# Performance work log

Hardware: AMD Instinct MI355X
Metric: run time of the kernel (lower is better)

## Reference

```python
import jax, jax.numpy as jnp
import numpy as np
from functools import partial

B, T, D = 4, 1024, 1024
NH = 16            # n_branches
DH = D // NH       # d_branch = 64
SOMA_H = int(D * 3.0)
EPS = 1e-5

def _gelu(x):
    return jax.nn.gelu(x, approximate=False)  # torch default GELU is exact erf

def _gconv(x_cf, w, b, pad_left, groups):
    # x_cf: [B, C_in, T], w: [C_out, C_in//groups, K] (torch OIW layout)
    y = jax.lax.conv_general_dilated(
        x_cf, w, window_strides=(1,), padding=[(pad_left, 0)],
        feature_group_count=groups, dimension_numbers=('NCH', 'OIH', 'NCH'))
    return y + b[None, :, None]

def setup_inputs() -> dict:
    key = jax.random.key(0)
    ks = jax.random.split(key, 16)
    s = 0.02
    return {
        'x': jax.random.normal(ks[0], (B, T, D), jnp.float32),
        'nmda': jax.random.normal(ks[1], (B, NH, DH), jnp.float32),
        'qkv_w': jax.random.normal(ks[2], (D, 3 * D), jnp.float32) * s,
        'nmda_decay': jax.random.normal(ks[3], (1, NH, 1, DH), jnp.float32) * 0.1 + 0.9,
        'tconv_w': jax.random.normal(ks[4], (D, DH, 5), jnp.float32) * s,
        'tconv_b': jnp.zeros((D,), jnp.float32),
        'ffu_w': jax.random.normal(ks[5], (2 * D, DH, 1), jnp.float32) * s,
        'ffu_b': jnp.zeros((2 * D,), jnp.float32),
        'ffd_w': jax.random.normal(ks[6], (D, 2 * DH, 1), jnp.float32) * s,
        'ffd_b': jnp.zeros((D,), jnp.float32),
        'gn_w': jnp.ones((D,), jnp.float32),
        'gn_b': jnp.zeros((D,), jnp.float32),
        'soma_w': jax.random.normal(ks[7], (D, D), jnp.float32) * s,
        'ln_w': jnp.ones((D,), jnp.float32),
        'ln_b': jnp.zeros((D,), jnp.float32),
        'w1': jax.random.normal(ks[8], (D, SOMA_H), jnp.float32) * s,
        'b1': jnp.zeros((SOMA_H,), jnp.float32),
        'w2': jax.random.normal(ks[9], (SOMA_H, D), jnp.float32) * s,
        'b2': jnp.zeros((D,), jnp.float32),
    }

def reference(x, nmda, qkv_w, nmda_decay, tconv_w, tconv_b, ffu_w, ffu_b,
              ffd_w, ffd_b, gn_w, gn_b, soma_w, ln_w, ln_b, w1, b1, w2, b2):
    # QKV projection -> [B, T, 3, NH, DH] -> Q,K,V [B, NH, T, DH]
    qkv = (x @ qkv_w).reshape(B, T, 3, NH, DH).transpose(2, 0, 3, 1, 4)
    Q, K, V = qkv[0], qkv[1], qkv[2]
    # NMDA trace injection into V, gated by sigmoid(decay)
    tau = jax.nn.sigmoid(nmda_decay)                    # [1, NH, 1, DH]
    V = V + nmda[:, :, None, :] * tau
    # causal SDPA
    scale = 1.0 / jnp.sqrt(jnp.asarray(DH, x.dtype))
    scores = jnp.einsum('bhqd,bhkd->bhqk', Q, K) * scale
    causal = jnp.tril(jnp.ones((T, T), bool))
    scores = jnp.where(causal[None, None], scores, jnp.finfo(x.dtype).min)
    attn = jnp.einsum('bhqk,bhkd->bhqd', jax.nn.softmax(scores, axis=-1), V)
    branch_flat = attn.transpose(0, 2, 1, 3).reshape(B, T, D)   # [B,T,D]
    # causal temporal grouped conv (pad=4, k=5, truncated to T => left-pad 4)
    x_cf = branch_flat.transpose(0, 2, 1)                       # [B,D,T]
    x_cf = x_cf + _gconv(x_cf, tconv_w, tconv_b, 4, NH)
    # grouped 1x1 FFN
    ff_hidden = _gelu(_gconv(x_cf, ffu_w, ffu_b, 0, NH))        # [B,2D,T]
    ff_out = _gconv(ff_hidden, ffd_w, ffd_b, 0, NH).transpose(0, 2, 1)
    residual = branch_flat + ff_out
    # GroupNorm over each branch's DH channels (per token)
    r = residual.reshape(B, T, NH, DH)
    mu = r.mean(-1, keepdims=True)
    var = ((r - mu) ** 2).mean(-1, keepdims=True)
    normed_heads = (r - mu) / jnp.sqrt(var + EPS)
    normed_heads = normed_heads * gn_w.reshape(NH, DH) + gn_b.reshape(NH, DH)
    normed = normed_heads.reshape(B, T, D)
    # NMDA state update from last token
    branch_last = normed_heads[:, -1]                           # [B,NH,DH]
    tau2 = jax.nn.sigmoid(nmda_decay[:, :, 0, :])               # [1,NH,DH]
    new_nmda = tau2 * nmda + (1.0 - tau2) * branch_last
    # soma projection + LN + FFN (exact GELU)
    soma = normed @ soma_w
    mu2 = soma.mean(-1, keepdims=True)
    var2 = ((soma - mu2) ** 2).mean(-1, keepdims=True)
    lns = (soma - mu2) / jnp.sqrt(var2 + EPS) * ln_w + ln_b
    soma = soma + (_gelu(lns @ w1 + b1) @ w2 + b2)
    return soma, new_nmda
```

## Files before the change

### kernel.cpp

```cpp
#include <hip/hip_runtime.h>
#include <math.h>

#define B_  4
#define T_  1024
#define D_  1024
#define NH_ 16
#define DH_ 64
#define SH_ 3072

typedef unsigned short u16;
typedef __attribute__((ext_vector_type(8))) short bf16x8;
typedef __attribute__((ext_vector_type(4))) float f32x4;
typedef __attribute__((ext_vector_type(4))) unsigned short u16x4;
typedef __attribute__((ext_vector_type(8))) unsigned short u16x8;

__device__ __forceinline__ float gelu_f(float x) {
    return 0.5f * x * (1.0f + erff(x * 0.70710678118654752440f));
}
__device__ __forceinline__ float sigm_f(float x) {
    return 1.0f / (1.0f + __expf(-x));
}
__device__ __forceinline__ u16 f2bf(float f) {
    unsigned u = __builtin_bit_cast(unsigned, f);
    return (u16)((u + 0x7FFFu + ((u >> 16) & 1u)) >> 16);
}

#define GLD16(gsrc, ldst) __builtin_amdgcn_global_load_lds( \
    (__attribute__((address_space(1))) void*)(gsrc),        \
    (__attribute__((address_space(3))) void*)(ldst), 16, 0, 0)

__global__ __launch_bounds__(256) void cast_bf16_k(
    const float* __restrict__ in, u16* __restrict__ out, int n8)
{
    int i = blockIdx.x * 256 + threadIdx.x;
    if (i >= n8) return;
    const float4* p = (const float4*)(in + (size_t)i * 8);
    float4 a = p[0], b = p[1];
    u16x8 o;
    o[0] = f2bf(a.x); o[1] = f2bf(a.y); o[2] = f2bf(a.z); o[3] = f2bf(a.w);
    o[4] = f2bf(b.x); o[5] = f2bf(b.y); o[6] = f2bf(b.z); o[7] = f2bf(b.w);
    *(u16x8*)(out + (size_t)i * 8) = o;
}

__global__ __launch_bounds__(256) void transpose_cast_k(
    const float* __restrict__ W, u16* __restrict__ Wt, int K, int N)
{
    __shared__ float t[32][33];
    const int n0 = blockIdx.x * 32, k0 = blockIdx.y * 32;
    const int tid = threadIdx.x;
    {
        int kr = tid >> 3, nc = (tid & 7) * 4;
        float4 v = *(const float4*)(W + (size_t)(k0 + kr) * N + n0 + nc);
        t[kr][nc] = v.x; t[kr][nc + 1] = v.y; t[kr][nc + 2] = v.z; t[kr][nc + 3] = v.w;
    }
    __syncthreads();
    {
        int nr = tid >> 3, kc = (tid & 7) * 4;
        u16x4 o = { f2bf(t[kc][nr]), f2bf(t[kc + 1][nr]),
                    f2bf(t[kc + 2][nr]), f2bf(t[kc + 3][nr]) };
        *(u16x4*)(Wt + (size_t)(n0 + nr) * K + k0 + kc) = o;
    }
}

template<bool BIAS, bool GELU, bool ACCUM, bool BF16OUT>
__global__ __launch_bounds__(256) void gemm_mfma(
    const u16* __restrict__ A, const u16* __restrict__ Bt,
    const float* __restrict__ bias, void* __restrict__ Cv,
    int M, int N, int K)
{
    __shared__ u16 As[4096];
    __shared__ u16 Bs[4096];
    const int tid = threadIdx.x;
    const int m0 = blockIdx.y * 128, n0 = blockIdx.x * 128;
    const int w = tid >> 6, l = tid & 63;
    const int mw = (w >> 1) * 64, nw = (w & 1) * 64;
    const int lr = l & 15, kg = l >> 4;
    const int swz = kg ^ ((lr >> 1) & 3);

    f32x4 acc[4][4];
#pragma unroll
    for (int i = 0; i < 4; ++i)
#pragma unroll
        for (int j = 0; j < 4; ++j) acc[i][j] = (f32x4){0.f, 0.f, 0.f, 0.f};

    const int mA0 = tid >> 2;
    const int kg0 = (tid & 3) ^ ((mA0 >> 1) & 3);
    const int mA1 = (256 + tid) >> 2;
    const int kg1 = ((256 + tid) & 3) ^ ((mA1 >> 1) & 3);
    const u16* a0 = A + (size_t)(m0 + mA0) * K + kg0 * 8;
    const u16* a1 = A + (size_t)(m0 + mA1) * K + kg1 * 8;
    const u16* b0 = Bt + (size_t)(n0 + mA0) * K + kg0 * 8;
    const u16* b1 = Bt + (size_t)(n0 + mA1) * K + kg1 * 8;
    u16* lA0 = As + tid * 8;  u16* lA1 = As + (256 + tid) * 8;
    u16* lB0 = Bs + tid * 8;  u16* lB1 = Bs + (256 + tid) * 8;

    for (int k0 = 0; k0 < K; k0 += 32) {
        __syncthreads();
        GLD16(a0 + k0, lA0); GLD16(a1 + k0, lA1);
        GLD16(b0 + k0, lB0); GLD16(b1 + k0, lB1);
        __syncthreads();

        bf16x8 aF[4], bF[4];
#pragma unroll
        for (int mt = 0; mt < 4; ++mt) {
            int row = mw + mt * 16 + lr;
            aF[mt] = *(const bf16x8*)&As[(row * 4 + swz) * 8];
            int rowb = nw + mt * 16 + lr;
            bF[mt] = *(const bf16x8*)&Bs[(rowb * 4 + swz) * 8];
        }
#pragma unroll
        for (int mt = 0; mt < 4; ++mt)
#pragma unroll
            for (int nt = 0; nt < 4; ++nt)
                acc[mt][nt] = __builtin_amdgcn_mfma_f32_16x16x32_bf16(
                    aF[mt], bF[nt], acc[mt][nt], 0, 0, 0);
    }

    const int lq = l >> 4;
#pragma unroll
    for (int mt = 0; mt < 4; ++mt) {
#pragma unroll
        for (int nt = 0; nt < 4; ++nt) {
            int row = m0 + mw + mt * 16 + lq * 4;
            int col = n0 + nw + nt * 16 + lr;
            float bsv = BIAS ? bias[col] : 0.f;
#pragma unroll
            for (int j = 0; j < 4; ++j) {
                float v = acc[mt][nt][j] + bsv;
                if (GELU) v = gelu_f(v);
                size_t idx = (size_t)(row + j) * N + col;
                if (BF16OUT) {
                    ((u16*)Cv)[idx] = f2bf(v);
                } else {
                    float* C = (float*)Cv;
                    if (ACCUM) v += C[idx];
                    C[idx] = v;
                }
            }
        }
    }
}

__global__ __launch_bounds__(256) void attn_mfma(
    const u16* __restrict__ qkv, const float* __restrict__ nmda,
    const float* __restrict__ nmda_decay, float* __restrict__ branch)
{
    const int qt = 15 - (int)blockIdx.x;
    const int h  = blockIdx.y;
    const int b  = blockIdx.z;
    const int tid = threadIdx.x;
    const int w  = tid >> 6, l = tid & 63;
    const int lr = l & 15, kg = l >> 4;
    const int q0 = qt * 64;

    __shared__ u16 Ks[64 * 64];
    __shared__ u16 Vrow[64 * 64];
    __shared__ u16 Vt[64 * 64];
    __shared__ u16 Ps[4][16 * 64];

    bf16x8 qf[2];
    {
        const u16* qrow = qkv + (size_t)(b * T_ + q0 + w * 16 + lr) * (3 * D_) + h * 64;
        qf[0] = *(const bf16x8*)(qrow + kg * 8);
        qf[1] = *(const bf16x8*)(qrow + 32 + kg * 8);
    }

    float nshift[4];
#pragma unroll
    for (int nt = 0; nt < 4; ++nt) {
        int d = nt * 16 + lr;
        nshift[nt] = nmda[(size_t)(b * NH_ + h) * 64 + d] * sigm_f(nmda_decay[h * 64 + d]);
    }

    f32x4 O[4];
#pragma unroll
    for (int nt = 0; nt < 4; ++nt) O[nt] = (f32x4){0.f, 0.f, 0.f, 0.f};
    float m_run[4] = {-INFINITY, -INFINITY, -INFINITY, -INFINITY};
    float l_run[4] = {0.f, 0.f, 0.f, 0.f};

    const int p0 = tid, p1 = 256 + tid;
    const int kr0 = p0 >> 3, ks0 = p0 & 7;
    const int kr1 = p1 >> 3, ks1 = p1 & 7;
    const u16* kbase = qkv + (size_t)(b * T_) * (3 * D_) + D_ + h * 64;
    const u16* vbase = kbase + D_;
    const u16* ksrc0 = kbase + (size_t)kr0 * (3 * D_) + ((ks0 ^ (kr0 & 7)) << 3);
    const u16* ksrc1 = kbase + (size_t)kr1 * (3 * D_) + ((ks1 ^ (kr1 & 7)) << 3);
    const u16* vsrc0 = vbase + (size_t)kr0 * (3 * D_) + (ks0 << 3);
    const u16* vsrc1 = vbase + (size_t)kr1 * (3 * D_) + (ks1 << 3);

    for (int kt = 0; kt <= qt; ++kt) {
        const size_t off = (size_t)(kt * 64) * (3 * D_);
        __syncthreads();
        GLD16(ksrc0 + off, Ks + p0 * 8);
        GLD16(ksrc1 + off, Ks + p1 * 8);
        GLD16(vsrc0 + off, Vrow + p0 * 8);
        GLD16(vsrc1 + off, Vrow + p1 * 8);
        __syncthreads();

        {
            const int d = l;
#pragma unroll
            for (int pp = 0; pp < 2; ++pp) {
                const int gk = w + pp * 4;
                u16x8 col;
#pragma unroll
                for (int j = 0; j < 8; ++j)
                    col[j] = Vrow[(gk * 8 + j) * 64 + d];
                *(u16x8*)&Vt[d * 64 + ((gk ^ (d & 7)) << 3)] = col;
            }
        }

        f32x4 s[4];
#pragma unroll
        for (int nt = 0; nt < 4; ++nt) s[nt] = (f32x4){0.f, 0.f, 0.f, 0.f};
#pragma unroll
        for (int ks = 0; ks < 2; ++ks) {
#pragma unroll
            for (int nt = 0; nt < 4; ++nt) {
                int krow = nt * 16 + lr;
                bf16x8 kf = *(const bf16x8*)&Ks[krow * 64 + (((ks * 4 + kg) ^ (krow & 7)) << 3)];
                s[nt] = __builtin_amdgcn_mfma_f32_16x16x32_bf16(qf[ks], kf, s[nt], 0, 0, 0);
            }
        }
#pragma unroll
        for (int nt = 0; nt < 4; ++nt)
#pragma unroll
            for (int j = 0; j < 4; ++j) s[nt][j] *= 0.125f;

        __syncthreads();

        if (kt == qt) {
#pragma unroll
            for (int nt = 0; nt < 4; ++nt) {
                int kvp = nt * 16 + lr;
#pragma unroll
                for (int j = 0; j < 4; ++j) {
                    int qp = w * 16 + kg * 4 + j;
                    if (kvp > qp) s[nt][j] = -INFINITY;
                }
            }
        }

        float c4[4];
#pragma unroll
        for (int j = 0; j < 4; ++j) {
            float mx = fmaxf(fmaxf(s[0][j], s[1][j]), fmaxf(s[2][j], s[3][j]));
#pragma unroll
            for (int msk = 1; msk < 16; msk <<= 1) mx = fmaxf(mx, __shfl_xor(mx, msk));
            float mn = fmaxf(m_run[j], mx);
            c4[j] = __expf(m_run[j] - mn);
            m_run[j] = mn;
            float ls = 0.f;
#pragma unroll
            for (int nt = 0; nt < 4; ++nt) {
                float p = __expf(s[nt][j] - mn);
                s[nt][j] = p;
                ls += p;
            }
#pragma unroll
            for (int msk = 1; msk < 16; msk <<= 1) ls += __shfl_xor(ls, msk);
            l_run[j] = l_run[j] * c4[j] + ls;
        }

#pragma unroll
        for (int nt = 0; nt < 4; ++nt) {
#pragma unroll
            for (int j = 0; j < 4; ++j) {
                int r = kg * 4 + j;
                int c = nt * 16 + lr;
                Ps[w][r * 64 + (((c >> 3) ^ (r & 7)) << 3) + (c & 7)] = f2bf(s[nt][j]);
            }
        }

#pragma unroll
        for (int nt = 0; nt < 4; ++nt)
#pragma unroll
            for (int j = 0; j < 4; ++j) O[nt][j] *= c4[j];
#pragma unroll
        for (int ks = 0; ks < 2; ++ks) {
            bf16x8 pa = *(const bf16x8*)&Ps[w][lr * 64 + (((ks * 4 + kg) ^ (lr & 7)) << 3)];
#pragma unroll
            for (int nt = 0; nt < 4; ++nt) {
                int vrow = nt * 16 + lr;
                bf16x8 vf = *(const bf16x8*)&Vt[vrow * 64 + (((ks * 4 + kg) ^ (vrow & 7)) << 3)];
                O[nt] = __builtin_amdgcn_mfma_f32_16x16x32_bf16(pa, vf, O[nt], 0, 0, 0);
            }
        }
    }

#pragma unroll
    for (int j = 0; j < 4; ++j) {
        float inv = 1.f / l_run[j];
        int qrow = q0 + w * 16 + kg * 4 + j;
        float* orow = branch + (size_t)(b * T_ + qrow) * D_ + h * 64;
#pragma unroll
        for (int nt = 0; nt < 4; ++nt)
            orow[nt * 16 + lr] = O[nt][j] * inv + nshift[nt];
    }
}

__global__ __launch_bounds__(256) void tconv_kernel(
    const float* __restrict__ branch, const float* __restrict__ w,
    const float* __restrict__ bias, float* __restrict__ xcf2)
{
    const int tid = threadIdx.x;
    const int t0 = blockIdx.x * 128;
    const int c0 = blockIdx.y * 16;
    const int b  = blockIdx.z;
    const int g  = c0 >> 6;
    __shared__ __align__(16) float xl[132][68];
    __shared__ __align__(16) float wl[16][5][64];
    __shared__ float bl[16];

    for (int idx = tid; idx < 132 * 16; idx += 256) {
        int tl = idx >> 4, q = (idx & 15) * 4;
        int tg = t0 - 4 + tl;
        float4 v = (tg >= 0)
            ? *(const float4*)&branch[(size_t)(b * T_ + tg) * D_ + g * 64 + q]
            : make_float4(0.f, 0.f, 0.f, 0.f);
        *(float4*)&xl[tl][q] = v;
    }
    for (int idx = tid; idx < 16 * 320; idx += 256) {
        int cc = idx / 320, r = idx - cc * 320;
        int i = r / 5, k = r - i * 5;
        wl[cc][k][i] = w[(size_t)(c0 + cc) * 320 + r];
    }
    if (tid < 16) bl[tid] = bias[c0 + tid];
    __syncthreads();

    const int t  = tid & 127;
    const int h8 = (tid >> 7) * 8;
    const int cl = (c0 & 63) + h8;

    float acc[8];
    {
        float4 s0 = *(const float4*)&xl[t + 4][cl];
        float4 s1 = *(const float4*)&xl[t + 4][cl + 4];
        acc[0] = s0.x + bl[h8 + 0]; acc[1] = s0.y + bl[h8 + 1];
        acc[2] = s0.z + bl[h8 + 2]; acc[3] = s0.w + bl[h8 + 3];
        acc[4] = s1.x + bl[h8 + 4]; acc[5] = s1.y + bl[h8 + 5];
        acc[6] = s1.z + bl[h8 + 6]; acc[7] = s1.w + bl[h8 + 7];
    }
#pragma unroll
    for (int k = 0; k < 5; ++k) {
        const float* xr = &xl[t + k][0];
#pragma unroll 4
        for (int i4 = 0; i4 < 16; ++i4) {
            float4 xv = *(const float4*)&xr[i4 * 4];
#pragma unroll
            for (int cc = 0; cc < 8; ++cc) {
                float4 w4 = *(const float4*)&wl[h8 + cc][k][i4 * 4];
                acc[cc] += xv.x * w4.x + xv.y * w4.y + xv.z * w4.z + xv.w * w4.w;
            }
        }
    }
    float* op = &xcf2[(size_t)(b * T_ + t0 + t) * D_ + c0 + h8];
    *(float4*)op       = make_float4(acc[0], acc[1], acc[2], acc[3]);
    *(float4*)(op + 4) = make_float4(acc[4], acc[5], acc[6], acc[7]);
}

__global__ __launch_bounds__(256) void ffu_kernel(
    const float* __restrict__ xcf2, const float* __restrict__ w,
    const float* __restrict__ bias, float* __restrict__ hid)
{
    const int tid = threadIdx.x;
    const int t0 = blockIdx.x * 64, g = blockIdx.y, b = blockIdx.z;
    __shared__ __align__(16) float al[64][68];
    __shared__ __align__(16) float wlds[64][132];

    for (int idx = tid; idx < 64 * 64; idx += 256) {
        int i = idx & 63, tl = idx >> 6;
        al[i][tl] = xcf2[(size_t)(b * T_ + t0 + tl) * D_ + g * 64 + i];
    }
    for (int idx = tid; idx < 128 * 64; idx += 256) {
        int i = idx & 63, o = idx >> 6;
        wlds[i][o] = w[(size_t)(g * 128 + o) * 64 + i];
    }
    __syncthreads();

    const int ot = (tid & 15) * 8;
    const int tt = (tid >> 4) * 4;
    float acc[4][8];
#pragma unroll
    for (int i = 0; i < 4; ++i)
#pragma unroll
        for (int j = 0; j < 8; ++j) acc[i][j] = 0.f;

#pragma unroll 8
    for (int i = 0; i < 64; ++i) {
        float4 a4 = *(const float4*)&al[i][tt];
        float4 w0 = *(const float4*)&wlds[i][ot];
        float4 w1 = *(const float4*)&wlds[i][ot + 4];
        float av[4] = {a4.x, a4.y, a4.z, a4.w};
        float wv[8] = {w0.x, w0.y, w0.z, w0.w, w1.x, w1.y, w1.z, w1.w};
#pragma unroll
        for (int ti = 0; ti < 4; ++ti)
#pragma unroll
            for (int oi = 0; oi < 8; ++oi)
                acc[ti][oi] = fmaf(av[ti], wv[oi], acc[ti][oi]);
    }

    float4 bb0 = *(const float4*)&bias[g * 128 + ot];
    float4 bb1 = *(const float4*)&bias[g * 128 + ot + 4];
    float bv[8] = {bb0.x, bb0.y, bb0.z, bb0.w, bb1.x, bb1.y, bb1.z, bb1.w};
#pragma unroll
    for (int ti = 0; ti < 4; ++ti) {
        float o_[8];
#pragma unroll
        for (int oi = 0; oi < 8; ++oi) o_[oi] = gelu_f(acc[ti][oi] + bv[oi]);
        float* hp = hid + (size_t)(b * T_ + t0 + tt + ti) * (2 * D_) + g * 128 + ot;
        *(float4*)hp       = make_float4(o_[0], o_[1], o_[2], o_[3]);
        *(float4*)(hp + 4) = make_float4(o_[4], o_[5], o_[6], o_[7]);
    }
}

__global__ __launch_bounds__(256) void ffd_gn_kernel(
    const float* __restrict__ hid, const float* __restrict__ w,
    const float* __restrict__ bias, const float* __restrict__ branch,
    const float* __restrict__ gn_w, const float* __restrict__ gn_b,
    const float* __restrict__ nmda, const float* __restrict__ nmda_decay,
    u16* __restrict__ normed, float* __restrict__ out_nmda)
{
    const int tid = threadIdx.x;
    const int t0 = blockIdx.x * 32, g = blockIdx.y, b = blockIdx.z;
    __shared__ __align__(16) float al[128][36];
    __shared__ __align__(16) float wl[128][68];

    for (int idx = tid; idx < 128 * 32; idx += 256) {
        int j = idx & 127, tl = idx >> 7;
        al[j][tl] = hid[(size_t)(b * T_ + t0 + tl) * (2 * D_) + g * 128 + j];
    }
    for (int idx = tid; idx < 64 * 128; idx += 256) {
        int j = idx & 127, c = idx >> 7;
        wl[j][c] = w[(size_t)(g * 64 + c) * 128 + j];
    }
    __syncthreads();

    const int c0 = (tid & 15) * 4;
    const int tt = (tid >> 4) * 2;
    float acc[2][4];
#pragma unroll
    for (int i = 0; i < 2; ++i)
#pragma unroll
        for (int j = 0; j < 4; ++j) acc[i][j] = 0.f;

#pragma unroll 8
    for (int j = 0; j < 128; ++j) {
        float2 a2 = *(const float2*)&al[j][tt];
        float4 w4 = *(const float4*)&wl[j][c0];
        acc[0][0] = fmaf(a2.x, w4.x, acc[0][0]);
        acc[0][1] = fmaf(a2.x, w4.y, acc[0][1]);
        acc[0][2] = fmaf(a2.x, w4.z, acc[0][2]);
        acc[0][3] = fmaf(a2.x, w4.w, acc[0][3]);
        acc[1][0] = fmaf(a2.y, w4.x, acc[1][0]);
        acc[1][1] = fmaf(a2.y, w4.y, acc[1][1]);
        acc[1][2] = fmaf(a2.y, w4.z, acc[1][2]);
        acc[1][3] = fmaf(a2.y, w4.w, acc[1][3]);
    }

    float4 bb = *(const float4*)&bias[g * 64 + c0];
    float4 gw = *(const float4*)&gn_w[g * 64 + c0];
    float4 gb = *(const float4*)&gn_b[g * 64 + c0];

#pragma unroll
    for (int tq = 0; tq < 2; ++tq) {
        const int tg = t0 + tt + tq;
        float4 br = *(const float4*)&branch[(size_t)(b * T_ + tg) * D_ + g * 64 + c0];
        float r0 = br.x + acc[tq][0] + bb.x;
        float r1 = br.y + acc[tq][1] + bb.y;
        float r2 = br.z + acc[tq][2] + bb.z;
        float r3 = br.w + acc[tq][3] + bb.w;
        float sm = r0 + r1 + r2 + r3;
#pragma unroll
        for (int m = 1; m < 16; m <<= 1) sm += __shfl_xor(sm, m);
        float mu = sm * (1.f / 64.f);
        float d0 = r0 - mu, d1 = r1 - mu, d2 = r2 - mu, d3 = r3 - mu;
        float vs = d0 * d0 + d1 * d1 + d2 * d2 + d3 * d3;
#pragma unroll
        for (int m = 1; m < 16; m <<= 1) vs += __shfl_xor(vs, m);
        float is = rsqrtf(vs * (1.f / 64.f) + 1e-5f);
        float n0 = d0 * is * gw.x + gb.x;
        float n1 = d1 * is * gw.y + gb.y;
        float n2 = d2 * is * gw.z + gb.z;
        float n3 = d3 * is * gw.w + gb.w;
        u16x4 o = { f2bf(n0), f2bf(n1), f2bf(n2), f2bf(n3) };
        *(u16x4*)&normed[(size_t)(b * T_ + tg) * D_ + g * 64 + c0] = o;
        if (tg == T_ - 1) {
            float nv[4] = {n0, n1, n2, n3};
#pragma unroll
            for (int cc = 0; cc < 4; ++cc) {
                int dloc = c0 + cc;
                int ni = (b * NH_ + g) * 64 + dloc;
                float t2 = sigm_f(nmda_decay[g * 64 + dloc]);
                out_nmda[ni] = t2 * nmda[ni] + (1.f - t2) * nv[cc];
            }
        }
    }
}

__global__ __launch_bounds__(256) void ln_kernel(
    const float* __restrict__ x, const float* __restrict__ w,
    const float* __restrict__ bo, u16* __restrict__ y)
{
    __shared__ float red[8];
    const int row = blockIdx.x, tid = threadIdx.x;
    const float* xr = x + (size_t)row * D_;
    float4 v = *(const float4*)&xr[tid * 4];
    float s = v.x + v.y + v.z + v.w;
#pragma unroll
    for (int m = 32; m; m >>= 1) s += __shfl_xor(s, m);
    if ((tid & 63) == 0) red[tid >> 6] = s;
    __syncthreads();
    float mu = (red[0] + red[1] + red[2] + red[3]) * (1.f / 1024.f);
    float dx = v.x - mu, dy = v.y - mu, dz = v.z - mu, dw = v.w - mu;
    float q = dx * dx + dy * dy + dz * dz + dw * dw;
#pragma unroll
    for (int m = 32; m; m >>= 1) q += __shfl_xor(q, m);
    if ((tid & 63) == 0) red[4 + (tid >> 6)] = q;
    __syncthreads();
    float var = (red[4] + red[5] + red[6] + red[7]) * (1.f / 1024.f);
    float is = rsqrtf(var + 1e-5f);
    float4 wv = *(const float4*)&w[tid * 4];
    float4 bv = *(const float4*)&bo[tid * 4];
    u16x4 o = { f2bf(dx * is * wv.x + bv.x), f2bf(dy * is * wv.y + bv.y),
                f2bf(dz * is * wv.z + bv.z), f2bf(dw * is * wv.w + bv.w) };
    *(u16x4*)&y[(size_t)row * D_ + tid * 4] = o;
}

extern "C" void kernel_launch(void* const* d_in, const int* in_sizes, int n_in,
                              void* d_out, int out_size, void* d_ws, size_t ws_size,
                              hipStream_t stream)
{
    const float* x       = (const float*)d_in[0];
    const float* nmda    = (const float*)d_in[1];
    const float* qkv_w   = (const float*)d_in[2];
    const float* nmda_d  = (const float*)d_in[3];
    const float* tconv_w = (const float*)d_in[4];
    const float* tconv_b = (const float*)d_in[5];
    const float* ffu_w   = (const float*)d_in[6];
    const float* ffu_b   = (const float*)d_in[7];
    const float* ffd_w   = (const float*)d_in[8];
    const float* ffd_b   = (const float*)d_in[9];
    const float* gn_w    = (const float*)d_in[10];
    const float* gn_b    = (const float*)d_in[11];
    const float* soma_w  = (const float*)d_in[12];
    const float* ln_w    = (const float*)d_in[13];
    const float* ln_b    = (const float*)d_in[14];
    const float* w1      = (const float*)d_in[15];
    const float* b1      = (const float*)d_in[16];
    const float* w2      = (const float*)d_in[17];
    const float* b2      = (const float*)d_in[18];
    (void)in_sizes; (void)n_in; (void)out_size; (void)ws_size;

    float* outp     = (float*)d_out;
    float* soma     = outp;
    float* out_nmda = outp + (size_t)B_ * T_ * D_;

    float* ws     = (float*)d_ws;
    float* branch = ws;
    float* xcf2   = ws + (size_t)4194304;
    float* normed = ws + (size_t)8388608;
    float* qkvb   = ws + (size_t)12582912;
    u16*   qkvbf = (u16*)qkvb;
    float* hid   = qkvb;
    u16*   h1bf  = (u16*)qkvb;

    u16* xbf    = (u16*)normed;
    u16* wqkvT  = (u16*)normed + 4194304;
    u16* normbf = (u16*)xcf2;
    u16* somaT  = (u16*)xcf2 + 4194304;
    u16* lnsbf  = (u16*)branch;
    u16* w1T    = (u16*)branch + 4194304;
    u16* w2T    = (u16*)xcf2;

    hipLaunchKernelGGL(cast_bf16_k, dim3(2048), dim3(256), 0, stream, x, xbf, 524288);
    hipLaunchKernelGGL(transpose_cast_k, dim3(96, 32), dim3(256), 0, stream,
                       qkv_w, wqkvT, 1024, 3072);
    hipLaunchKernelGGL((gemm_mfma<false, false, false, true>), dim3(24, 32), dim3(256), 0, stream,
                       xbf, wqkvT, nullptr, qkvbf, 4096, 3072, 1024);
    hipLaunchKernelGGL(attn_mfma, dim3(16, NH_, B_), dim3(256), 0, stream,
                       qkvbf, nmda, nmda_d, branch);
    hipLaunchKernelGGL(tconv_kernel, dim3(8, 64, 4), dim3(256), 0, stream,
                       branch, tconv_w, tconv_b, xcf2);
    hipLaunchKernelGGL(ffu_kernel, dim3(16, NH_, B_), dim3(256), 0, stream,
                       xcf2, ffu_w, ffu_b, hid);
    hipLaunchKernelGGL(ffd_gn_kernel, dim3(32, NH_, B_), dim3(256), 0, stream,
                       hid, ffd_w, ffd_b, branch, gn_w, gn_b, nmda, nmda_d,
                       normbf, out_nmda);
    hipLaunchKernelGGL(transpose_cast_k, dim3(32, 32), dim3(256), 0, stream,
                       soma_w, somaT, 1024, 1024);
    hipLaunchKernelGGL((gemm_mfma<false, false, false, false>), dim3(8, 32), dim3(256), 0, stream,
                       normbf, somaT, nullptr, soma, 4096, 1024, 1024);
    hipLaunchKernelGGL(ln_kernel, dim3(B_ * T_), dim3(256), 0, stream,
                       soma, ln_w, ln_b, lnsbf);
    hipLaunchKernelGGL(transpose_cast_k, dim3(96, 32), dim3(256), 0, stream,
                       w1, w1T, 1024, 3072);
    hipLaunchKernelGGL((gemm_mfma<true, true, false, true>), dim3(24, 32), dim3(256), 0, stream,
                       lnsbf, w1T, b1, h1bf, 4096, 3072, 1024);
    hipLaunchKernelGGL(transpose_cast_k, dim3(32, 96), dim3(256), 0, stream,
                       w2, w2T, 3072, 1024);
    hipLaunchKernelGGL((gemm_mfma<true, false, true, false>), dim3(8, 32), dim3(256), 0, stream,
                       h1bf, w2T, b2, soma, 4096, 1024, 3072);
}
```

Measured before the change: 548.4 us.

## Rewrite grouped temporal conv as bf16 MFMA implicit GEMM with prepped weights

Replaces the fp32 scalar grouped causal conv with an implicit-GEMM kernel that uses bf16 16x16x32 MFMA instructions. A new prep kernel reorders the conv weights into a K-major bf16 layout, and the activations are converted to bf16 into swizzled LDS on load. Each block now covers a whole 64-channel group across 128 timesteps instead of 16 channels. This trades fp32 precision in the conv for matrix-core throughput and adds one extra small kernel launch.

```diff
diff --git a/kernel.cpp b/kernel.cpp
--- a/kernel.cpp
+++ b/kernel.cpp
@@ -60,6 +60,15 @@
                     f2bf(t[kc + 2][nr]), f2bf(t[kc + 3][nr]) };
         *(u16x4*)(Wt + (size_t)(n0 + nr) * K + k0 + kc) = o;
     }
+}
+
+__global__ __launch_bounds__(256) void tconv_wprep(
+    const float* __restrict__ w, u16* __restrict__ Wtp)
+{
+    int idx = blockIdx.x * 256 + threadIdx.x;
+    int c = idx / 320, r = idx - c * 320;
+    int k5 = r >> 6, i = r & 63;
+    Wtp[idx] = f2bf(w[c * 320 + i * 5 + k5]);
 }
 
 template<bool BIAS, bool GELU, bool ACCUM, bool BF16OUT>
@@ -299,64 +308,92 @@
     }
 }
 
-__global__ __launch_bounds__(256) void tconv_kernel(
-    const float* __restrict__ branch, const float* __restrict__ w,
+__global__ __launch_bounds__(256) void tconv_mfma(
+    const float* __restrict__ branch, const u16* __restrict__ Wtp,
     const float* __restrict__ bias, float* __restrict__ xcf2)
 {
     const int tid = threadIdx.x;
     const int t0 = blockIdx.x * 128;
-    const int c0 = blockIdx.y * 16;
+    const int g  = blockIdx.y;
     const int b  = blockIdx.z;
-    const int g  = c0 >> 6;
-    __shared__ __align__(16) float xl[132][68];
-    __shared__ __align__(16) float wl[16][5][64];
-    __shared__ float bl[16];
-
-    for (int idx = tid; idx < 132 * 16; idx += 256) {
-        int tl = idx >> 4, q = (idx & 15) * 4;
-        int tg = t0 - 4 + tl;
-        float4 v = (tg >= 0)
-            ? *(const float4*)&branch[(size_t)(b * T_ + tg) * D_ + g * 64 + q]
-            : make_float4(0.f, 0.f, 0.f, 0.f);
-        *(float4*)&xl[tl][q] = v;
-    }
-    for (int idx = tid; idx < 16 * 320; idx += 256) {
-        int cc = idx / 320, r = idx - cc * 320;
-        int i = r / 5, k = r - i * 5;
-        wl[cc][k][i] = w[(size_t)(c0 + cc) * 320 + r];
-    }
-    if (tid < 16) bl[tid] = bias[c0 + tid];
-    __syncthreads();
-
-    const int t  = tid & 127;
-    const int h8 = (tid >> 7) * 8;
-    const int cl = (c0 & 63) + h8;
-
-    float acc[8];
-    {
-        float4 s0 = *(const float4*)&xl[t + 4][cl];
-        float4 s1 = *(const float4*)&xl[t + 4][cl + 4];
-        acc[0] = s0.x + bl[h8 + 0]; acc[1] = s0.y + bl[h8 + 1];
-        acc[2] = s0.z + bl[h8 + 2]; acc[3] = s0.w + bl[h8 + 3];
-        acc[4] = s1.x + bl[h8 + 4]; acc[5] = s1.y + bl[h8 + 5];
-        acc[6] = s1.z + bl[h8 + 6]; acc[7] = s1.w + bl[h8 + 7];
-    }
-#pragma unroll
-    for (int k = 0; k < 5; ++k) {
-        const float* xr = &xl[t + k][0];
-#pragma unroll 4
-        for (int i4 = 0; i4 < 16; ++i4) {
-            float4 xv = *(const float4*)&xr[i4 * 4];
-#pragma unroll
-            for (int cc = 0; cc < 8; ++cc) {
-                float4 w4 = *(const float4*)&wl[h8 + cc][k][i4 * 4];
-                acc[cc] += xv.x * w4.x + xv.y * w4.y + xv.z * w4.z + xv.w * w4.w;
-            }
-        }
-    }
-    float* op = &xcf2[(size_t)(b * T_ + t0 + t) * D_ + c0 + h8];
-    *(float4*)op       = make_float4(acc[0], acc[1], acc[2], acc[3]);
-    *(float4*)(op + 4) = make_float4(acc[4], acc[5], acc[6], acc[7]);
+    const int w = tid >> 6, l = tid & 63;
+    const int lr = l & 15, kg = l >> 4;
+    const int mw = (w >> 1) * 64;
+    const int nw = (w & 1) * 32;
+
+    __shared__ u16 xbf[132 * 64];
+    __shared__ u16 Bs[64 * 32];
+
+    for (int idx = tid; idx < 132 * 8; idx += 256) {
+        int row = idx >> 3, gr = idx & 7;
+        int tg = t0 - 4 + row;
+        u16x8 v8 = (u16x8){0, 0, 0, 0, 0, 0, 0, 0};
+        if (tg >= 0) {
+            const float* src = &branch[(size_t)(b * T_ + tg) * D_ + g * 64 + gr * 8];
+            float4 f0 = *(const float4*)src;
+            float4 f1 = *(const float4*)(src + 4);
+            v8[0] = f2bf(f0.x); v8[1] = f2bf(f0.y); v8[2] = f2bf(f0.z); v8[3] = f2bf(f0.w);
+            v8[4] = f2bf(f1.x); v8[5] = f2bf(f1.y); v8[6] = f2bf(f1.z); v8[7] = f2bf(f1.w);
+        }
+        *(u16x8*)&xbf[row * 64 + ((gr ^ (row & 7)) << 3)] = v8;
+    }
+
+    f32x4 acc[4][2];
+#pragma unroll
+    for (int i = 0; i < 4; ++i)
+#pragma unroll
+        for (int j = 0; j < 2; ++j) acc[i][j] = (f32x4){0.f, 0.f, 0.f, 0.f};
+
+    const int mB  = tid >> 2;
+    const int kgb = (tid & 3) ^ ((mB >> 1) & 3);
+    const u16* bsrc = Wtp + (size_t)(g * 64 + mB) * 320 + kgb * 8;
+    u16* lB = Bs + tid * 8;
+    const int swzB = kg ^ ((lr >> 1) & 3);
+
+    for (int k0 = 0; k0 < 320; k0 += 32) {
+        __syncthreads();
+        GLD16(bsrc + k0, lB);
+        __syncthreads();
+
+        const int kgr = (k0 >> 3) + kg;
+        const int k5  = kgr >> 3;
+        const int ig  = kgr & 7;
+
+        bf16x8 aF[4];
+#pragma unroll
+        for (int mt = 0; mt < 4; ++mt) {
+            int row = mw + mt * 16 + lr + k5;
+            aF[mt] = *(const bf16x8*)&xbf[row * 64 + ((ig ^ (row & 7)) << 3)];
+        }
+        bf16x8 bF[2];
+#pragma unroll
+        for (int nt = 0; nt < 2; ++nt) {
+            int rb = nw + nt * 16 + lr;
+            bF[nt] = *(const bf16x8*)&Bs[(rb * 4 + swzB) * 8];
+        }
+#pragma unroll
+        for (int mt = 0; mt < 4; ++mt)
+#pragma unroll
+            for (int nt = 0; nt < 2; ++nt)
+                acc[mt][nt] = __builtin_amdgcn_mfma_f32_16x16x32_bf16(
+                    aF[mt], bF[nt], acc[mt][nt], 0, 0, 0);
+    }
+
+    const int lq = l >> 4;
+#pragma unroll
+    for (int mt = 0; mt < 4; ++mt) {
+#pragma unroll
+        for (int nt = 0; nt < 2; ++nt) {
+            int trow = t0 + mw + mt * 16 + lq * 4;
+            int col  = g * 64 + nw + nt * 16 + lr;
+            float bv = bias[col];
+#pragma unroll
+            for (int j = 0; j < 4; ++j) {
+                size_t idx = (size_t)(b * T_ + trow + j) * D_ + col;
+                xcf2[idx] = acc[mt][nt][j] + bv + branch[idx];
+            }
+        }
+    }
 }
 
 __global__ __launch_bounds__(256) void ffu_kernel(
@@ -567,12 +604,14 @@
 
     u16* xbf    = (u16*)normed;
     u16* wqkvT  = (u16*)normed + 4194304;
+    u16* Wtp    = (u16*)normed + 7340032;
     u16* normbf = (u16*)xcf2;
     u16* somaT  = (u16*)xcf2 + 4194304;
     u16* lnsbf  = (u16*)branch;
     u16* w1T    = (u16*)branch + 4194304;
     u16* w2T    = (u16*)xcf2;
 
+    hipLaunchKernelGGL(tconv_wprep, dim3(1280), dim3(256), 0, stream, tconv_w, Wtp);
     hipLaunchKernelGGL(cast_bf16_k, dim3(2048), dim3(256), 0, stream, x, xbf, 524288);
     hipLaunchKernelGGL(transpose_cast_k, dim3(96, 32), dim3(256), 0, stream,
                        qkv_w, wqkvT, 1024, 3072);
@@ -580,8 +619,8 @@
                        xbf, wqkvT, nullptr, qkvbf, 4096, 3072, 1024);
     hipLaunchKernelGGL(attn_mfma, dim3(16, NH_, B_), dim3(256), 0, stream,
                        qkvbf, nmda, nmda_d, branch);
-    hipLaunchKernelGGL(tconv_kernel, dim3(8, 64, 4), dim3(256), 0, stream,
-                       branch, tconv_w, tconv_b, xcf2);
+    hipLaunchKernelGGL(tconv_mfma, dim3(8, NH_, B_), dim3(256), 0, stream,
+                       branch, Wtp, tconv_b, xcf2);
     hipLaunchKernelGGL(ffu_kernel, dim3(16, NH_, B_), dim3(256), 0, stream,
                        xcf2, ffu_w, ffu_b, hid);
     hipLaunchKernelGGL(ffd_gn_kernel, dim3(32, NH_, B_), dim3(256), 0, stream,
```

New measurement: 489.7 us. 10.7% less time.
